# Kernel optimization log

Measured on AMD Instinct MI355X. Metric: run time of the kernel, lower is better.

Reference implementation:

```python
import math
import jax, jax.numpy as jnp
import numpy as np

EPS = 1e-12
NHEAD = 12
HEAD_DIM = 64  # d_model // nhead = 768 // 12


def setup_inputs() -> dict:
    key = jax.random.key(0)
    ks = jax.random.split(key, 8)
    L, D, H = 12, 768, 2048
    B, S = 8, 1024
    std = 0.02
    return {
        "x": jax.random.normal(ks[0], (B, S, D), jnp.float32),
        "wq": jax.random.normal(ks[1], (L, D, D), jnp.float32) * std,
        "wk": jax.random.normal(ks[2], (L, D, D), jnp.float32) * std,
        "wv": jax.random.normal(ks[3], (L, D, D), jnp.float32) * std,
        "wo": jax.random.normal(ks[4], (L, D, D), jnp.float32) * std,
        "w1": jax.random.normal(ks[5], (L, H, D), jnp.float32) * std,
        "w2": jax.random.normal(ks[6], (L, D, H), jnp.float32) * std,
        "attn_norm_w": jnp.ones((L, D), jnp.float32),
        "ffn_norm_w": jnp.ones((L, D), jnp.float32),
    }


def _rmsnorm(x, w):
    # x * rsqrt(mean(x^2) + eps) * w
    return x * jax.lax.rsqrt(jnp.mean(x * x, axis=-1, keepdims=True) + EPS) * w


def _block(x, params):
    wq, wk, wv, wo, w1, w2, anw, fnw = params
    B, S, D = x.shape
    # --- attention (manual matmul-softmax-matmul, fp32 softmax) ---
    xn = _rmsnorm(x, anw)
    q = jnp.einsum('bsd,ed->bse', xn, wq).reshape(B, S, NHEAD, HEAD_DIM)
    k = jnp.einsum('bsd,ed->bse', xn, wk).reshape(B, S, NHEAD, HEAD_DIM)
    v = jnp.einsum('bsd,ed->bse', xn, wv).reshape(B, S, NHEAD, HEAD_DIM)
    scores = jnp.einsum('bqhd,bkhd->bhqk', q, k) / math.sqrt(HEAD_DIM)
    probs = jax.nn.softmax(scores.astype(jnp.float32), axis=-1).astype(x.dtype)
    attn = jnp.einsum('bhqk,bkhd->bqhd', probs, v).reshape(B, S, D)
    h = x + jnp.einsum('bsd,ed->bse', attn, wo)
    # --- FFN: w2(silu(w1(h_norm))) ---
    hn = _rmsnorm(h, fnw)
    ff = jnp.einsum('bsh,dh->bsd', jax.nn.silu(jnp.einsum('bsd,hd->bsh', hn, w1)), w2)
    return h + ff


def reference(x, wq, wk, wv, wo, w1, w2, attn_norm_w, ffn_norm_w):
    def step(carry, p):
        return _block(carry, p), None
    out, _ = jax.lax.scan(step, x, (wq, wk, wv, wo, w1, w2, attn_norm_w, ffn_norm_w))
    return out
```

## Files before the change

kernel.cpp:

```cpp
#include <hip/hip_runtime.h>
#include <stdint.h>

typedef unsigned short u16;
typedef unsigned int u32;
typedef __bf16 bf16x8 __attribute__((ext_vector_type(8)));
typedef float f32x4 __attribute__((ext_vector_type(4)));

__device__ __forceinline__ u16 f2bf(float f) {
  u32 u = __builtin_bit_cast(u32, f);
  u32 r = (u + 0x7FFFu + ((u >> 16) & 1u)) >> 16;
  return (u16)r;
}

__global__ __launch_bounds__(256)
void convert_w(const float* __restrict__ wq, const float* __restrict__ wk,
               const float* __restrict__ wv, const float* __restrict__ wo,
               const float* __restrict__ w1, const float* __restrict__ w2,
               u16* __restrict__ out) {
  size_t i = ((size_t)blockIdx.x * 256 + threadIdx.x) * 4;
  if (i >= 5505024) return;
  const float* src; size_t off;
  if (i < 589824)       { src = wq; off = i; }
  else if (i < 1179648) { src = wk; off = i - 589824; }
  else if (i < 1769472) { src = wv; off = i - 1179648; }
  else if (i < 2359296) { src = wo; off = i - 1769472; }
  else if (i < 3932160) { src = w1; off = i - 2359296; }
  else                  { src = w2; off = i - 3932160; }
  float4 v = *(const float4*)(src + off);
  u32 lo = (u32)f2bf(v.x) | ((u32)f2bf(v.y) << 16);
  u32 hi = (u32)f2bf(v.z) | ((u32)f2bf(v.w) << 16);
  *(uint2*)(out + i) = make_uint2(lo, hi);
}

__device__ __forceinline__ void rn_store4(u16* p, float4 v, float4 w, float sc) {
  u32 lo = (u32)f2bf(v.x * sc * w.x) | ((u32)f2bf(v.y * sc * w.y) << 16);
  u32 hi = (u32)f2bf(v.z * sc * w.z) | ((u32)f2bf(v.w * sc * w.w) << 16);
  *(uint2*)p = make_uint2(lo, hi);
}

__global__ __launch_bounds__(256)
void rmsnorm_k(const float* __restrict__ x, const float* __restrict__ w,
               u16* __restrict__ out) {
  const int tok = (blockIdx.x << 2) + (threadIdx.x >> 6);
  const int l = threadIdx.x & 63;
  const float* xr = x + (size_t)tok * 768;
  float4 v0 = *(const float4*)(xr + l * 4);
  float4 v1 = *(const float4*)(xr + 256 + l * 4);
  float4 v2 = *(const float4*)(xr + 512 + l * 4);
  float ss = v0.x*v0.x + v0.y*v0.y + v0.z*v0.z + v0.w*v0.w
           + v1.x*v1.x + v1.y*v1.y + v1.z*v1.z + v1.w*v1.w
           + v2.x*v2.x + v2.y*v2.y + v2.z*v2.z + v2.w*v2.w;
  ss += __shfl_xor(ss, 1);  ss += __shfl_xor(ss, 2);  ss += __shfl_xor(ss, 4);
  ss += __shfl_xor(ss, 8);  ss += __shfl_xor(ss, 16); ss += __shfl_xor(ss, 32);
  float sc = rsqrtf(ss * (1.f / 768.f) + 1e-12f);
  float4 w0 = *(const float4*)(w + l * 4);
  float4 w1v = *(const float4*)(w + 256 + l * 4);
  float4 w2v = *(const float4*)(w + 512 + l * 4);
  u16* o = out + (size_t)tok * 768;
  rn_store4(o + l * 4, v0, w0, sc);
  rn_store4(o + 256 + l * 4, v1, w1v, sc);
  rn_store4(o + 512 + l * 4, v2, w2v, sc);
}

#define GEMM_CORE(A_, W_, K_, m0_, n0_)                                             \
  for (int kt = 0; kt < (K_); kt += 64) {                                           \
    __syncthreads();                                                                \
    _Pragma("unroll")                                                               \
    for (int ii = 0; ii < 4; ++ii) {                                                \
      int issue = (w << 2) + ii;                                                    \
      int r = (issue << 3) + (l >> 3);                                              \
      int c = (l & 7) ^ (r & 7);                                                    \
      __builtin_amdgcn_global_load_lds((A_) + (size_t)((m0_) + r) * (K_) + kt + c * 8, \
                                       As + issue * 512, 16, 0, 0);                 \
      __builtin_amdgcn_global_load_lds((W_) + (size_t)((n0_) + r) * (K_) + kt + c * 8, \
                                       Ws + issue * 512, 16, 0, 0);                 \
    }                                                                               \
    __syncthreads();                                                                \
    _Pragma("unroll")                                                               \
    for (int kc = 0; kc < 2; ++kc) {                                                \
      int chunk = lg + (kc << 2);                                                   \
      bf16x8 af[4], bfr[4];                                                         \
      _Pragma("unroll")                                                             \
      for (int i = 0; i < 4; ++i) {                                                 \
        int mr = (wm << 6) + (i << 4) + ll;                                         \
        af[i] = *(const bf16x8*)((const char*)As + mr * 128 + ((chunk ^ (mr & 7)) << 4)); \
        int nr = (wn << 6) + (i << 4) + ll;                                         \
        bfr[i] = *(const bf16x8*)((const char*)Ws + nr * 128 + ((chunk ^ (nr & 7)) << 4)); \
      }                                                                             \
      _Pragma("unroll")                                                             \
      for (int i = 0; i < 4; ++i)                                                   \
        _Pragma("unroll")                                                           \
        for (int j = 0; j < 4; ++j)                                                 \
          acc[i][j] = __builtin_amdgcn_mfma_f32_16x16x32_bf16(af[i], bfr[j], acc[i][j], 0, 0, 0); \
    }                                                                               \
  }

template<int EP>
__global__ __launch_bounds__(256, 2)
void gemm_bt(const u16* __restrict__ A, const u16* __restrict__ W,
             void* __restrict__ outp, const float* __restrict__ Res,
             int M, int N, int K) {
  __shared__ __align__(16) u16 As[128 * 64];
  __shared__ __align__(16) u16 Ws[128 * 64];
  const int tid = threadIdx.x;
  const int w = tid >> 6, l = tid & 63;
  const int lg = l >> 4, ll = l & 15;
  const int ntiles = N >> 7;
  const int mt = blockIdx.x / ntiles, nt = blockIdx.x - mt * ntiles;
  const int m0 = mt << 7, n0 = nt << 7;
  const int wm = w >> 1, wn = w & 1;

  const f32x4 fz = {0.f, 0.f, 0.f, 0.f};
  f32x4 acc[4][4];
#pragma unroll
  for (int i = 0; i < 4; ++i)
#pragma unroll
    for (int j = 0; j < 4; ++j) acc[i][j] = fz;

  GEMM_CORE(A, W, K, m0, n0)

  const int g4 = lg << 2;
#pragma unroll
  for (int i = 0; i < 4; ++i) {
#pragma unroll
    for (int j = 0; j < 4; ++j) {
      int row0 = m0 + (wm << 6) + (i << 4) + g4;
      int col = n0 + (wn << 6) + (j << 4) + ll;
      f32x4 v = acc[i][j];
      if (EP == 0) {
        u16* o = (u16*)outp;
#pragma unroll
        for (int e = 0; e < 4; ++e) o[(size_t)(row0 + e) * N + col] = f2bf(v[e]);
      } else if (EP == 1) {
        float* o = (float*)outp;
#pragma unroll
        for (int e = 0; e < 4; ++e) {
          size_t idx = (size_t)(row0 + e) * N + col;
          o[idx] = Res[idx] + v[e];
        }
      } else {
        u16* o = (u16*)outp;
#pragma unroll
        for (int e = 0; e < 4; ++e) {
          float xx = v[e];
          o[(size_t)(row0 + e) * N + col] = f2bf(xx / (1.f + __expf(-xx)));
        }
      }
    }
  }
}

__global__ __launch_bounds__(256, 4)
void gemm_bt64(const u16* __restrict__ A, const u16* __restrict__ W,
               float* __restrict__ outp, const float* __restrict__ Res,
               int M, int N, int K) {
  __shared__ __align__(16) u16 As[64 * 64];
  __shared__ __align__(16) u16 Ws[128 * 64];
  const int tid = threadIdx.x;
  const int w = tid >> 6, l = tid & 63;
  const int lg = l >> 4, ll = l & 15;
  const int ntiles = N >> 7;
  const int mt = blockIdx.x / ntiles, nt = blockIdx.x - mt * ntiles;
  const int m0 = mt << 6, n0 = nt << 7;
  const int wm = w >> 1, wn = w & 1;

  const f32x4 fz = {0.f, 0.f, 0.f, 0.f};
  f32x4 acc[2][4];
#pragma unroll
  for (int i = 0; i < 2; ++i)
#pragma unroll
    for (int j = 0; j < 4; ++j) acc[i][j] = fz;

  for (int kt = 0; kt < K; kt += 64) {
    __syncthreads();
#pragma unroll
    for (int ii = 0; ii < 6; ++ii) {
      int issue = w * 6 + ii;
      if (issue < 8) {
        int r = (issue << 3) + (l >> 3);
        int c = (l & 7) ^ (r & 7);
        __builtin_amdgcn_global_load_lds(A + (size_t)(m0 + r) * K + kt + c * 8,
                                         As + issue * 512, 16, 0, 0);
      } else {
        int is2 = issue - 8;
        int r = (is2 << 3) + (l >> 3);
        int c = (l & 7) ^ (r & 7);
        __builtin_amdgcn_global_load_lds(W + (size_t)(n0 + r) * K + kt + c * 8,
                                         Ws + is2 * 512, 16, 0, 0);
      }
    }
    __syncthreads();
#pragma unroll
    for (int kc = 0; kc < 2; ++kc) {
      int chunk = lg + (kc << 2);
      bf16x8 af[2], bfr[4];
#pragma unroll
      for (int i = 0; i < 2; ++i) {
        int mr = (wm << 5) + (i << 4) + ll;
        af[i] = *(const bf16x8*)((const char*)As + mr * 128 + ((chunk ^ (mr & 7)) << 4));
      }
#pragma unroll
      for (int j = 0; j < 4; ++j) {
        int nr = (wn << 6) + (j << 4) + ll;
        bfr[j] = *(const bf16x8*)((const char*)Ws + nr * 128 + ((chunk ^ (nr & 7)) << 4));
      }
#pragma unroll
      for (int i = 0; i < 2; ++i)
#pragma unroll
        for (int j = 0; j < 4; ++j)
          acc[i][j] = __builtin_amdgcn_mfma_f32_16x16x32_bf16(af[i], bfr[j], acc[i][j], 0, 0, 0);
    }
  }

  const int g4 = lg << 2;
#pragma unroll
  for (int i = 0; i < 2; ++i) {
#pragma unroll
    for (int j = 0; j < 4; ++j) {
      int row0 = m0 + (wm << 5) + (i << 4) + g4;
      int col = n0 + (wn << 6) + (j << 4) + ll;
      f32x4 v = acc[i][j];
#pragma unroll
      for (int e = 0; e < 4; ++e) {
        size_t idx = (size_t)(row0 + e) * N + col;
        outp[idx] = Res[idx] + v[e];
      }
    }
  }
}

__global__ __launch_bounds__(256, 2)
void gemm_qkv(const u16* __restrict__ A, const u16* __restrict__ W,
              u16* __restrict__ Qo, u16* __restrict__ Ko, u16* __restrict__ Vo) {
  __shared__ __align__(16) u16 As[128 * 64];
  __shared__ __align__(16) u16 Ws[128 * 64];
  const int tid = threadIdx.x;
  const int w = tid >> 6, l = tid & 63;
  const int lg = l >> 4, ll = l & 15;
  const int mt = blockIdx.x / 18, nt = blockIdx.x - mt * 18;
  const int m0 = mt << 7, n0 = nt << 7;
  const int wm = w >> 1, wn = w & 1;
  const int K = 768;

  const f32x4 fz = {0.f, 0.f, 0.f, 0.f};
  f32x4 acc[4][4];
#pragma unroll
  for (int i = 0; i < 4; ++i)
#pragma unroll
    for (int j = 0; j < 4; ++j) acc[i][j] = fz;

  GEMM_CORE(A, W, K, m0, n0)

  const int g4 = lg << 2;
#pragma unroll
  for (int i = 0; i < 4; ++i) {
#pragma unroll
    for (int j = 0; j < 4; ++j) {
      int row0 = m0 + (wm << 6) + (i << 4) + g4;
      int col = n0 + (wn << 6) + (j << 4) + ll;
      f32x4 v = acc[i][j];
      if (nt < 12) {
        u16* o = (nt < 6) ? Qo : Ko;
        int c = (nt < 6) ? col : (col - 768);
#pragma unroll
        for (int e = 0; e < 4; ++e) o[(size_t)(row0 + e) * 768 + c] = f2bf(v[e]);
      } else {
        int c = col - 1536;
        int vrow = ((row0 >> 10) * 768) + c;
        u32 lo = (u32)f2bf(v[0]) | ((u32)f2bf(v[1]) << 16);
        u32 hi = (u32)f2bf(v[2]) | ((u32)f2bf(v[3]) << 16);
        *(uint2*)(Vo + ((size_t)vrow << 10) + (row0 & 1023)) = make_uint2(lo, hi);
      }
    }
  }
}

__global__ __launch_bounds__(256, 2)
void attn_kernel(const u16* __restrict__ Q, const u16* __restrict__ Kg,
                 const u16* __restrict__ Vt, u16* __restrict__ Og) {
  __shared__ __align__(16) u16 Ks[128 * 64];
  __shared__ __align__(16) u16 Vs[64 * 128];
  __shared__ __align__(16) __bf16 Ps[4][16 * 128];
  __shared__ float red[4][32];

  const int tid = threadIdx.x;
  const int w = tid >> 6, l = tid & 63;
  const int lg = l >> 4, ll = l & 15;
  const int bid = blockIdx.x;
  const int qt = bid & 7, bh = bid >> 3;
  const int b = bh / 12, hh = bh - b * 12;
  const float SC = 0.125f * 1.44269504f;

  bf16x8 qf[2][2];
  {
    const int tq = (b << 10) + (qt << 7) + (w << 5);
#pragma unroll
    for (int fm = 0; fm < 2; ++fm)
#pragma unroll
      for (int kc = 0; kc < 2; ++kc)
        qf[fm][kc] = *(const bf16x8*)(Q + (size_t)(tq + fm * 16 + ll) * 768 + hh * 64 + kc * 32 + lg * 8);
  }

  const f32x4 fz = {0.f, 0.f, 0.f, 0.f};
  f32x4 oacc[4][2];
#pragma unroll
  for (int i = 0; i < 4; ++i) { oacc[i][0] = fz; oacc[i][1] = fz; }
  float mrow[2][4], lrow[2][4];
#pragma unroll
  for (int fm = 0; fm < 2; ++fm)
#pragma unroll
    for (int j = 0; j < 4; ++j) { mrow[fm][j] = -1e30f; lrow[fm][j] = 0.f; }

  for (int kt = 0; kt < 8; ++kt) {
    __syncthreads();
#pragma unroll
    for (int ii = 0; ii < 4; ++ii) {
      int issue = (w << 2) + ii;
      int r = (issue << 3) + (l >> 3);
      int c = (l & 7) ^ (r & 7);
      __builtin_amdgcn_global_load_lds(
          Kg + (size_t)((b << 10) + (kt << 7) + r) * 768 + hh * 64 + c * 8,
          Ks + issue * 512, 16, 0, 0);
      int rv = (issue << 2) + (l >> 4);
      int cv = ll ^ (rv & 7);
      __builtin_amdgcn_global_load_lds(
          Vt + (size_t)((bh << 6) + rv) * 1024 + (kt << 7) + cv * 8,
          Vs + issue * 512, 16, 0, 0);
    }
    __syncthreads();

    f32x4 sa[2][8];
#pragma unroll
    for (int fm = 0; fm < 2; ++fm)
#pragma unroll
      for (int fn = 0; fn < 8; ++fn) sa[fm][fn] = fz;
#pragma unroll
    for (int kc = 0; kc < 2; ++kc) {
      int chunk = lg + (kc << 2);
      bf16x8 kb[8];
#pragma unroll
      for (int fn = 0; fn < 8; ++fn) {
        int nr = (fn << 4) + ll;
        kb[fn] = *(const bf16x8*)((const char*)Ks + nr * 128 + ((chunk ^ (nr & 7)) << 4));
      }
#pragma unroll
      for (int fm = 0; fm < 2; ++fm)
#pragma unroll
        for (int fn = 0; fn < 8; ++fn)
          sa[fm][fn] = __builtin_amdgcn_mfma_f32_16x16x32_bf16(qf[fm][kc], kb[fn], sa[fm][fn], 0, 0, 0);
    }
#pragma unroll
    for (int fm = 0; fm < 2; ++fm)
#pragma unroll
      for (int fn = 0; fn < 8; ++fn) sa[fm][fn] *= SC;

#pragma unroll
    for (int fm = 0; fm < 2; ++fm) {
#pragma unroll
      for (int j = 0; j < 4; ++j) {
        float mx = sa[fm][0][j];
#pragma unroll
        for (int fn = 1; fn < 8; ++fn) mx = fmaxf(mx, sa[fm][fn][j]);
        mx = fmaxf(mx, __shfl_xor(mx, 1));
        mx = fmaxf(mx, __shfl_xor(mx, 2));
        mx = fmaxf(mx, __shfl_xor(mx, 4));
        mx = fmaxf(mx, __shfl_xor(mx, 8));
        float mold = mrow[fm][j];
        float mnew = fmaxf(mold, mx);
        float scal = __builtin_amdgcn_exp2f(mold - mnew);
        float rs = 0.f;
        int rq = (lg << 2) + j;
#pragma unroll
        for (int fn = 0; fn < 8; ++fn) {
          float p = __builtin_amdgcn_exp2f(sa[fm][fn][j] - mnew);
          rs += p;
          int kk = (fn << 4) + ll;
          Ps[w][rq * 128 + (((kk >> 3) ^ (rq & 7)) << 3) + (kk & 7)] = (__bf16)p;
        }
        rs += __shfl_xor(rs, 1); rs += __shfl_xor(rs, 2);
        rs += __shfl_xor(rs, 4); rs += __shfl_xor(rs, 8);
        lrow[fm][j] = lrow[fm][j] * scal + rs;
        mrow[fm][j] = mnew;
        if (ll == 0) red[w][rq] = scal;
      }

      asm volatile("" ::: "memory");

      float s0 = red[w][ll];
#pragma unroll
      for (int fd = 0; fd < 4; ++fd) oacc[fd][fm] *= s0;

#pragma unroll
      for (int ch = 0; ch < 4; ++ch) {
        int chunk = lg + (ch << 2);
        int qr = ll;
        bf16x8 pb = *(const bf16x8*)((const char*)&Ps[w][0] + qr * 256 + ((chunk ^ (qr & 7)) << 4));
#pragma unroll
        for (int fd = 0; fd < 4; ++fd) {
          int dr = (fd << 4) + ll;
          bf16x8 av = *(const bf16x8*)((const char*)Vs + dr * 256 + ((chunk ^ (dr & 7)) << 4));
          oacc[fd][fm] = __builtin_amdgcn_mfma_f32_16x16x32_bf16(av, pb, oacc[fd][fm], 0, 0, 0);
        }
      }

      asm volatile("" ::: "memory");
    }
  }

#pragma unroll
  for (int fm = 0; fm < 2; ++fm)
#pragma unroll
    for (int j = 0; j < 4; ++j)
      if (ll == 0) red[w][(fm << 4) + (lg << 2) + j] = lrow[fm][j];
  asm volatile("" ::: "memory");
  float inv0 = 1.f / red[w][ll];
  float inv1 = 1.f / red[w][16 + ll];
  const int tq0 = (b << 10) + (qt << 7) + (w << 5);
#pragma unroll
  for (int fd = 0; fd < 4; ++fd) {
#pragma unroll
    for (int fo = 0; fo < 2; ++fo) {
      int q = (fo << 4) + ll;
      float inv = fo ? inv1 : inv0;
      f32x4 v = oacc[fd][fo];
      int d0 = (fd << 4) + (lg << 2);
      u16* o = Og + (size_t)(tq0 + q) * 768 + hh * 64 + d0;
      u32 lo = (u32)f2bf(v[0] * inv) | ((u32)f2bf(v[1] * inv) << 16);
      u32 hi = (u32)f2bf(v[2] * inv) | ((u32)f2bf(v[3] * inv) << 16);
      *(uint2*)o = make_uint2(lo, hi);
    }
  }
}

extern "C" void kernel_launch(void* const* d_in, const int* in_sizes, int n_in,
                              void* d_out, int out_size, void* d_ws, size_t ws_size,
                              hipStream_t stream) {
  const float* x = (const float*)d_in[0];
  const float* wq = (const float*)d_in[1];
  const float* wk = (const float*)d_in[2];
  const float* wv = (const float*)d_in[3];
  const float* wo = (const float*)d_in[4];
  const float* w1 = (const float*)d_in[5];
  const float* w2 = (const float*)d_in[6];
  const float* anw = (const float*)d_in[7];
  const float* fnw = (const float*)d_in[8];

  char* ws = (char*)d_ws;
  float* h    = (float*)(ws);
  u16* xn     = (u16*)(ws + 25165824);
  u16* qb     = (u16*)(ws + 37748736);
  u16* kb     = (u16*)(ws + 50331648);
  u16* vt     = (u16*)(ws + 62914560);
  u16* ff1    = (u16*)(ws + 75497472);
  u16* wbuf   = (u16*)(ws + 109051904);

  hipMemcpyAsync(h, x, 25165824, hipMemcpyDeviceToDevice, stream);

  for (int L = 0; L < 12; ++L) {
    convert_w<<<5376, 256, 0, stream>>>(
        wq + (size_t)L * 589824, wk + (size_t)L * 589824,
        wv + (size_t)L * 589824, wo + (size_t)L * 589824,
        w1 + (size_t)L * 1572864, w2 + (size_t)L * 1572864, wbuf);
    rmsnorm_k<<<2048, 256, 0, stream>>>(h, anw + L * 768, xn);
    gemm_qkv<<<1152, 256, 0, stream>>>(xn, wbuf, qb, kb, vt);
    attn_kernel<<<768, 256, 0, stream>>>(qb, kb, vt, qb);
    gemm_bt64<<<768, 256, 0, stream>>>(qb, wbuf + 1769472, h, h, 8192, 768, 768);
    rmsnorm_k<<<2048, 256, 0, stream>>>(h, fnw + L * 768, xn);
    gemm_bt<2><<<1024, 256, 0, stream>>>(xn, wbuf + 2359296, ff1, nullptr, 8192, 2048, 768);
    float* outw = (L == 11) ? (float*)d_out : h;
    gemm_bt64<<<768, 256, 0, stream>>>(ff1, wbuf + 3932160, outw, h, 8192, 768, 2048);
  }
}
```

Before: 3.012 ms.

## Transpose QK^T MFMA so each lane owns a query row in softmax

Swaps the MFMA operand order so the score tile is transposed, giving each lane a single query row across its four accumulator elements. Row max and sum then reduce mostly in registers with only two cross-lane shuffles. The per-row rescale factor no longer goes through shared memory, and P is written to LDS as 4-wide vectors instead of scalar stores. The block index mapping also changes so blocks with the same query tile but different batch/head are adjacent in launch order.

```diff
diff --git a/kernel.cpp b/kernel.cpp
--- a/kernel.cpp
+++ b/kernel.cpp
@@ -4,6 +4,7 @@
 typedef unsigned short u16;
 typedef unsigned int u32;
 typedef __bf16 bf16x8 __attribute__((ext_vector_type(8)));
+typedef __bf16 bf16x4 __attribute__((ext_vector_type(4)));
 typedef float f32x4 __attribute__((ext_vector_type(4)));
 
 __device__ __forceinline__ u16 f2bf(float f) {
@@ -281,13 +282,13 @@
   __shared__ __align__(16) u16 Ks[128 * 64];
   __shared__ __align__(16) u16 Vs[64 * 128];
   __shared__ __align__(16) __bf16 Ps[4][16 * 128];
-  __shared__ float red[4][32];
 
   const int tid = threadIdx.x;
   const int w = tid >> 6, l = tid & 63;
   const int lg = l >> 4, ll = l & 15;
   const int bid = blockIdx.x;
-  const int qt = bid & 7, bh = bid >> 3;
+  const int qt = bid / 96;
+  const int bh = bid - qt * 96;
   const int b = bh / 12, hh = bh - b * 12;
   const float SC = 0.125f * 1.44269504f;
 
@@ -305,11 +306,8 @@
   f32x4 oacc[4][2];
 #pragma unroll
   for (int i = 0; i < 4; ++i) { oacc[i][0] = fz; oacc[i][1] = fz; }
-  float mrow[2][4], lrow[2][4];
-#pragma unroll
-  for (int fm = 0; fm < 2; ++fm)
-#pragma unroll
-    for (int j = 0; j < 4; ++j) { mrow[fm][j] = -1e30f; lrow[fm][j] = 0.f; }
+  float mrow2[2] = {-1e30f, -1e30f};
+  float lrow2[2] = {0.f, 0.f};
 
   for (int kt = 0; kt < 8; ++kt) {
     __syncthreads();
@@ -347,7 +345,7 @@
       for (int fm = 0; fm < 2; ++fm)
 #pragma unroll
         for (int fn = 0; fn < 8; ++fn)
-          sa[fm][fn] = __builtin_amdgcn_mfma_f32_16x16x32_bf16(qf[fm][kc], kb[fn], sa[fm][fn], 0, 0, 0);
+          sa[fm][fn] = __builtin_amdgcn_mfma_f32_16x16x32_bf16(kb[fn], qf[fm][kc], sa[fm][fn], 0, 0, 0);
     }
 #pragma unroll
     for (int fm = 0; fm < 2; ++fm)
@@ -356,39 +354,41 @@
 
 #pragma unroll
     for (int fm = 0; fm < 2; ++fm) {
-#pragma unroll
-      for (int j = 0; j < 4; ++j) {
-        float mx = sa[fm][0][j];
-#pragma unroll
-        for (int fn = 1; fn < 8; ++fn) mx = fmaxf(mx, sa[fm][fn][j]);
-        mx = fmaxf(mx, __shfl_xor(mx, 1));
-        mx = fmaxf(mx, __shfl_xor(mx, 2));
-        mx = fmaxf(mx, __shfl_xor(mx, 4));
-        mx = fmaxf(mx, __shfl_xor(mx, 8));
-        float mold = mrow[fm][j];
-        float mnew = fmaxf(mold, mx);
-        float scal = __builtin_amdgcn_exp2f(mold - mnew);
-        float rs = 0.f;
-        int rq = (lg << 2) + j;
-#pragma unroll
-        for (int fn = 0; fn < 8; ++fn) {
-          float p = __builtin_amdgcn_exp2f(sa[fm][fn][j] - mnew);
-          rs += p;
-          int kk = (fn << 4) + ll;
-          Ps[w][rq * 128 + (((kk >> 3) ^ (rq & 7)) << 3) + (kk & 7)] = (__bf16)p;
-        }
-        rs += __shfl_xor(rs, 1); rs += __shfl_xor(rs, 2);
-        rs += __shfl_xor(rs, 4); rs += __shfl_xor(rs, 8);
-        lrow[fm][j] = lrow[fm][j] * scal + rs;
-        mrow[fm][j] = mnew;
-        if (ll == 0) red[w][rq] = scal;
-      }
+      f32x4 vm = sa[fm][0];
+#pragma unroll
+      for (int fn = 1; fn < 8; ++fn) {
+#pragma unroll
+        for (int e = 0; e < 4; ++e) vm[e] = fmaxf(vm[e], sa[fm][fn][e]);
+      }
+      float mx = fmaxf(fmaxf(vm[0], vm[1]), fmaxf(vm[2], vm[3]));
+      mx = fmaxf(mx, __shfl_xor(mx, 16));
+      mx = fmaxf(mx, __shfl_xor(mx, 32));
+      float mnew = fmaxf(mrow2[fm], mx);
+      float scal = __builtin_amdgcn_exp2f(mrow2[fm] - mnew);
+
+      f32x4 vsum = fz;
+#pragma unroll
+      for (int fn = 0; fn < 8; ++fn) {
+        f32x4 p;
+#pragma unroll
+        for (int e = 0; e < 4; ++e) p[e] = __builtin_amdgcn_exp2f(sa[fm][fn][e] - mnew);
+        vsum += p;
+        bf16x4 pv4;
+#pragma unroll
+        for (int e = 0; e < 4; ++e) pv4[e] = (__bf16)p[e];
+        int chunk = (fn << 1) + (lg >> 1);
+        *(bf16x4*)((char*)&Ps[w][0] + ll * 256 + ((chunk ^ (ll & 7)) << 4) + ((lg & 1) << 3)) = pv4;
+      }
+      float rs = (vsum[0] + vsum[1]) + (vsum[2] + vsum[3]);
+      rs += __shfl_xor(rs, 16);
+      rs += __shfl_xor(rs, 32);
+      lrow2[fm] = lrow2[fm] * scal + rs;
+      mrow2[fm] = mnew;
 
       asm volatile("" ::: "memory");
 
-      float s0 = red[w][ll];
-#pragma unroll
-      for (int fd = 0; fd < 4; ++fd) oacc[fd][fm] *= s0;
+#pragma unroll
+      for (int fd = 0; fd < 4; ++fd) oacc[fd][fm] *= scal;
 
 #pragma unroll
       for (int ch = 0; ch < 4; ++ch) {
@@ -407,14 +407,8 @@
     }
   }
 
-#pragma unroll
-  for (int fm = 0; fm < 2; ++fm)
-#pragma unroll
-    for (int j = 0; j < 4; ++j)
-      if (ll == 0) red[w][(fm << 4) + (lg << 2) + j] = lrow[fm][j];
-  asm volatile("" ::: "memory");
-  float inv0 = 1.f / red[w][ll];
-  float inv1 = 1.f / red[w][16 + ll];
+  float inv0 = 1.f / lrow2[0];
+  float inv1 = 1.f / lrow2[1];
   const int tq0 = (b << 10) + (qt << 7) + (w << 5);
 #pragma unroll
   for (int fd = 0; fd < 4; ++fd) {
```

Result: faster. 2.653 ms (-11.9%).
